# Optimization experiments

Measured on AMD Instinct MI355X. Metric: run time of the kernel, lower is better.

## Reference

```python
import jax, jax.numpy as jnp
import numpy as np

THETA = 10000.0
R_TOK = 4  # region_token_num


def _local_positions(regions, max_n):
    # 0-based position of each token within its region (count of prior tokens
    # with the same region id) -- order-based, works for any region layout.
    onehot = jax.nn.one_hot(regions, max_n + 1, dtype=jnp.int32)  # [B,T,N+1]
    counts = jnp.cumsum(onehot, axis=1)                            # inclusive
    return jnp.take_along_axis(counts, regions[..., None], axis=-1)[..., 0] - 1


def _rope(q, k, pos, theta):
    # full-head-dim rotary embedding, split-half convention
    D = q.shape[-1]
    inv_freq = 1.0 / (theta ** (jnp.arange(0, D, 2, dtype=jnp.float32) / D))  # [D/2]
    ang = pos[..., None].astype(jnp.float32) * inv_freq                        # [B,S,D/2]
    cos = jnp.tile(jnp.cos(ang), (1, 1, 2))[:, None]                           # [B,1,S,D]
    sin = jnp.tile(jnp.sin(ang), (1, 1, 2))[:, None]

    def rot(x):
        h = x.shape[-1] // 2
        return jnp.concatenate([-x[..., h:], x[..., :h]], axis=-1)

    return q * cos + rot(q) * sin, k * cos + rot(k) * sin


def setup_inputs() -> dict:
    B, H, D = 2, 16, 64
    T, MAX_N = 2048, 64
    P = MAX_N * R_TOK
    key = jax.random.key(0)
    ks = jax.random.split(key, 7)
    f = lambda k, s: jax.random.normal(k, s, dtype=jnp.float32)
    regions = jnp.sort(jax.random.randint(ks[6], (B, T), 1, MAX_N + 1, dtype=jnp.int32), axis=-1)
    return {
        'pool_q': f(ks[0], (B, H, P, D)),
        'pool_k': f(ks[1], (B, H, P, D)),
        'pool_v': f(ks[2], (B, H, P, D)),
        'x_q': f(ks[3], (B, H, T, D)),
        'x_k': f(ks[4], (B, H, T, D)),
        'x_v': f(ks[5], (B, H, T, D)),
        'regions': regions,
        't_mask': jnp.ones((B, T), dtype=bool),
        'n_mask': jnp.ones((B, MAX_N), dtype=bool),
        'max_n': MAX_N,
    }


def reference(pool_q, pool_k, pool_v, x_q, x_k, x_v, regions, t_mask, n_mask, max_n):
    B, H, P, D = pool_q.shape
    R = R_TOK
    # sequence = [pool, x]
    q = jnp.concatenate([pool_q, x_q], axis=2)
    k = jnp.concatenate([pool_k, x_k], axis=2)
    v = jnp.concatenate([pool_v, x_v], axis=2)

    # local-mode positions (use_pool_offset=False -> pool tokens at pos 0)
    pool_pos = jnp.zeros((B, P), dtype=jnp.int32)
    x_pos = (_local_positions(regions, max_n) + R) * (regions > 0).astype(jnp.int32)
    pos = jnp.concatenate([pool_pos, x_pos], axis=-1)  # [B,S]
    q, k = _rope(q, k, pos, THETA)

    # block-local (same-region) mask: [B,1,S,S], True = allowed
    pool_region = jnp.broadcast_to(jnp.repeat(jnp.arange(1, max_n + 1, dtype=jnp.int32), R)[None], (B, P))
    pool_valid = jnp.repeat(n_mask, R, axis=1)                      # [B,P]
    full_region = jnp.concatenate([pool_region, regions], axis=-1)  # [B,S]
    full_valid = jnp.concatenate([pool_valid, t_mask], axis=-1)     # [B,S]
    same = full_region[:, :, None] == full_region[:, None, :]
    valid = full_valid[:, :, None] & full_valid[:, None, :]
    nonpad = (full_region != 0)[:, :, None] & (full_region != 0)[:, None, :]
    mask = (same & valid & nonpad)[:, None]                          # [B,1,S,S]

    scores = jnp.einsum('bhqd,bhkd->bhqk', q, k) / jnp.sqrt(jnp.float32(D))
    scores = jnp.where(mask, scores, jnp.float32(-1e9))
    attn = jax.nn.softmax(scores, axis=-1)
    out = jnp.einsum('bhqk,bhkd->bhqd', attn, v)
    return out[:, :, :P, :]
```

## Files before the change

### kernel.cpp

```cpp
#include <hip/hip_runtime.h>

#define BB   2
#define HH   16
#define DD   64
#define TT   2048
#define MAXN 64
#define RTOK 4
#define PP   (MAXN * RTOK)
#define STR  72

typedef unsigned short u16x8 __attribute__((ext_vector_type(8)));
typedef unsigned short u16x4 __attribute__((ext_vector_type(4)));

__device__ __forceinline__ unsigned short f2bf(float f) {
    unsigned u = __float_as_uint(f);
    u += 0x7FFFu + ((u >> 16) & 1u);
    return (unsigned short)(u >> 16);
}
__device__ __forceinline__ float bf2f(unsigned short u) {
    return __uint_as_float(((unsigned int)u) << 16);
}

__global__ __launch_bounds__(256)
void build_ranges(const int* __restrict__ regions, int* __restrict__ tab) {
    const int b   = blockIdx.x;
    const int tid = threadIdx.x;
    const int* reg = regions + b * TT;
    int* t = tab + b * 66;
    const int i0 = tid * 8;
    int v[9];
    const int4 a0 = *(const int4*)(reg + i0);
    const int4 a1 = *(const int4*)(reg + i0 + 4);
    v[0] = a0.x; v[1] = a0.y; v[2] = a0.z; v[3] = a0.w;
    v[4] = a1.x; v[5] = a1.y; v[6] = a1.z; v[7] = a1.w;
    v[8] = (tid == 255) ? (MAXN + 1) : reg[i0 + 8];
    if (tid == 0)
        for (int rr = 1; rr <= v[0]; ++rr) t[rr] = 0;
    #pragma unroll
    for (int j = 0; j < 8; ++j)
        for (int rr = v[j] + 1; rr <= v[j + 1]; ++rr) t[rr] = i0 + j + 1;
}

__global__ __launch_bounds__(128, 4)
void lapd_attn(const float* __restrict__ pool_q,
               const float* __restrict__ pool_k,
               const float* __restrict__ pool_v,
               const float* __restrict__ x_k,
               const float* __restrict__ x_v,
               const int* __restrict__ tab,
               float* __restrict__ out) {
    const int blk   = blockIdx.x;
    const int r_idx = blk & (MAXN - 1);
    const int bh    = blk >> 6;
    const int b     = bh / HH;
    const int tid   = threadIdx.x;
    const int wave  = tid >> 6;
    const int lane  = tid & 63;

    __shared__ __align__(16) unsigned short k_s16[64][STR];
    __shared__ __align__(16) unsigned short v_t16[64][STR];
    __shared__ __align__(16) unsigned short p_s16[4][STR];
    __shared__ float q_s[4][DD];

    const int* tb    = tab + b * 66;
    const int start  = tb[r_idx + 1];
    const int cnt    = tb[r_idx + 2] - start;
    const int sstart = (cnt > 0) ? start : 0;

    const size_t poolbase = ((size_t)bh * PP + r_idx * RTOK) * DD;
    const float* pk = pool_k + poolbase;
    const float* pv = pool_v + poolbase;
    const float* xk = x_k + (size_t)bh * TT * DD;
    const float* xv = x_v + (size_t)bh * TT * DD;

    {
        const int r = lane >> 4, c = (lane & 15) * 4;
        const float4 q4 = *(const float4*)(pool_q + poolbase + (size_t)(r * DD) + c);
        *(float4*)&q_s[r][c] =
            make_float4(q4.x * 0.125f, q4.y * 0.125f, q4.z * 0.125f, q4.w * 0.125f);
    }

    const int g = lane >> 3;
    const int d = (lane & 7) * 4;
    float invf[4];
    #pragma unroll
    for (int c = 0; c < 4; ++c)
        invf[c] = __expf((float)(d + c) * (-9.210340371976184f / 32.0f));

    const int sk = lane & 31;
    const int h  = lane >> 5;
    const int row = 2 * wave + (lane >> 5);
    const int dp  = (lane & 31) * 2;

    float accA = 0.0f, accB = 0.0f, l = 0.0f;
    int xbase = 0;
    bool first = true;

    for (;;) {
        const int koff = first ? RTOK : 0;
        int nx = cnt - xbase;
        if (nx > 64 - koff) nx = 64 - koff;
        if (nx < 0) nx = 0;
        const int tn   = koff + nx;
        const int kmax = (tn + 7) & ~7;

        __syncthreads();

        #pragma unroll
        for (int ph = 0; ph < 2; ++ph) {
            const int base = 32 * wave + 16 * ph;
            if (base < tn) {
                const int keyA = base + 2 * g;
                const int keyB = keyA + 1;
                int xiA = keyA - koff; if (xiA > nx - 1) xiA = nx - 1; if (xiA < 0) xiA = 0;
                int xiB = keyB - koff; if (xiB > nx - 1) xiB = nx - 1; if (xiB < 0) xiB = 0;
                const bool pA = first && (keyA < RTOK);
                const bool pB = first && (keyB < RTOK);
                const float* kbA = pA ? (pk + keyA * DD) : (xk + (size_t)(sstart + xbase + xiA) * DD);
                const float* vbA = pA ? (pv + keyA * DD) : (xv + (size_t)(sstart + xbase + xiA) * DD);
                const float* kbB = pB ? (pk + keyB * DD) : (xk + (size_t)(sstart + xbase + xiB) * DD);
                const float* vbB = pB ? (pv + keyB * DD) : (xv + (size_t)(sstart + xbase + xiB) * DD);
                const float4 kA0 = *(const float4*)(kbA + d);
                const float4 kA1 = *(const float4*)(kbA + d + 32);
                const float4 vA0 = *(const float4*)(vbA + d);
                const float4 vA1 = *(const float4*)(vbA + d + 32);
                const float4 kB0 = *(const float4*)(kbB + d);
                const float4 kB1 = *(const float4*)(kbB + d + 32);
                const float4 vB0 = *(const float4*)(vbB + d);
                const float4 vB1 = *(const float4*)(vbB + d + 32);

                {
                    float lo0 = kA0.x, lo1 = kA0.y, lo2 = kA0.z, lo3 = kA0.w;
                    float hi0 = kA1.x, hi1 = kA1.y, hi2 = kA1.z, hi3 = kA1.w;
                    if (!pA) {
                        const float pos = (float)(xbase + xiA + RTOK);
                        float sv, cv;
                        __sincosf(pos * invf[0], &sv, &cv);
                        { const float L = lo0, H = hi0; lo0 = L*cv - H*sv; hi0 = H*cv + L*sv; }
                        __sincosf(pos * invf[1], &sv, &cv);
                        { const float L = lo1, H = hi1; lo1 = L*cv - H*sv; hi1 = H*cv + L*sv; }
                        __sincosf(pos * invf[2], &sv, &cv);
                        { const float L = lo2, H = hi2; lo2 = L*cv - H*sv; hi2 = H*cv + L*sv; }
                        __sincosf(pos * invf[3], &sv, &cv);
                        { const float L = lo3, H = hi3; lo3 = L*cv - H*sv; hi3 = H*cv + L*sv; }
                    }
                    u16x4 wlo = {f2bf(lo0), f2bf(lo1), f2bf(lo2), f2bf(lo3)};
                    u16x4 whi = {f2bf(hi0), f2bf(hi1), f2bf(hi2), f2bf(hi3)};
                    *(u16x4*)&k_s16[keyA][d]      = wlo;
                    *(u16x4*)&k_s16[keyA][d + 32] = whi;
                }
                {
                    float lo0 = kB0.x, lo1 = kB0.y, lo2 = kB0.z, lo3 = kB0.w;
                    float hi0 = kB1.x, hi1 = kB1.y, hi2 = kB1.z, hi3 = kB1.w;
                    if (!pB) {
                        const float pos = (float)(xbase + xiB + RTOK);
                        float sv, cv;
                        __sincosf(pos * invf[0], &sv, &cv);
                        { const float L = lo0, H = hi0; lo0 = L*cv - H*sv; hi0 = H*cv + L*sv; }
                        __sincosf(pos * invf[1], &sv, &cv);
                        { const float L = lo1, H = hi1; lo1 = L*cv - H*sv; hi1 = H*cv + L*sv; }
                        __sincosf(pos * invf[2], &sv, &cv);
                        { const float L = lo2, H = hi2; lo2 = L*cv - H*sv; hi2 = H*cv + L*sv; }
                        __sincosf(pos * invf[3], &sv, &cv);
                        { const float L = lo3, H = hi3; lo3 = L*cv - H*sv; hi3 = H*cv + L*sv; }
                    }
                    u16x4 wlo = {f2bf(lo0), f2bf(lo1), f2bf(lo2), f2bf(lo3)};
                    u16x4 whi = {f2bf(hi0), f2bf(hi1), f2bf(hi2), f2bf(hi3)};
                    *(u16x4*)&k_s16[keyB][d]      = wlo;
                    *(u16x4*)&k_s16[keyB][d + 32] = whi;
                }
                {
                    const unsigned w0 = (unsigned)f2bf(vA0.x) | ((unsigned)f2bf(vB0.x) << 16);
                    const unsigned w1 = (unsigned)f2bf(vA0.y) | ((unsigned)f2bf(vB0.y) << 16);
                    const unsigned w2 = (unsigned)f2bf(vA0.z) | ((unsigned)f2bf(vB0.z) << 16);
                    const unsigned w3 = (unsigned)f2bf(vA0.w) | ((unsigned)f2bf(vB0.w) << 16);
                    const unsigned h0 = (unsigned)f2bf(vA1.x) | ((unsigned)f2bf(vB1.x) << 16);
                    const unsigned h1 = (unsigned)f2bf(vA1.y) | ((unsigned)f2bf(vB1.y) << 16);
                    const unsigned h2 = (unsigned)f2bf(vA1.z) | ((unsigned)f2bf(vB1.z) << 16);
                    const unsigned h3 = (unsigned)f2bf(vA1.w) | ((unsigned)f2bf(vB1.w) << 16);
                    *(unsigned*)&v_t16[d + 0][keyA]  = w0;
                    *(unsigned*)&v_t16[d + 1][keyA]  = w1;
                    *(unsigned*)&v_t16[d + 2][keyA]  = w2;
                    *(unsigned*)&v_t16[d + 3][keyA]  = w3;
                    *(unsigned*)&v_t16[d + 32][keyA] = h0;
                    *(unsigned*)&v_t16[d + 33][keyA] = h1;
                    *(unsigned*)&v_t16[d + 34][keyA] = h2;
                    *(unsigned*)&v_t16[d + 35][keyA] = h3;
                }
            }
        }

        if (32 * wave < tn) {
            const int key = 32 * wave + sk;
            const int d0  = h * 32;
            float s0 = 0, s1 = 0, s2 = 0, s3 = 0;
            #pragma unroll
            for (int dd2 = 0; dd2 < 32; dd2 += 8) {
                const u16x8 kk = *(const u16x8*)&k_s16[key][d0 + dd2];
                const float k0 = bf2f(kk[0]), k1 = bf2f(kk[1]), k2 = bf2f(kk[2]), k3 = bf2f(kk[3]);
                const float k4 = bf2f(kk[4]), k5 = bf2f(kk[5]), k6 = bf2f(kk[6]), k7 = bf2f(kk[7]);
                const float4 qa0 = *(const float4*)&q_s[0][d0 + dd2];
                const float4 qb0 = *(const float4*)&q_s[0][d0 + dd2 + 4];
                const float4 qa1 = *(const float4*)&q_s[1][d0 + dd2];
                const float4 qb1 = *(const float4*)&q_s[1][d0 + dd2 + 4];
                const float4 qa2 = *(const float4*)&q_s[2][d0 + dd2];
                const float4 qb2 = *(const float4*)&q_s[2][d0 + dd2 + 4];
                const float4 qa3 = *(const float4*)&q_s[3][d0 + dd2];
                const float4 qb3 = *(const float4*)&q_s[3][d0 + dd2 + 4];
                s0 += qa0.x*k0 + qa0.y*k1 + qa0.z*k2 + qa0.w*k3 + qb0.x*k4 + qb0.y*k5 + qb0.z*k6 + qb0.w*k7;
                s1 += qa1.x*k0 + qa1.y*k1 + qa1.z*k2 + qa1.w*k3 + qb1.x*k4 + qb1.y*k5 + qb1.z*k6 + qb1.w*k7;
                s2 += qa2.x*k0 + qa2.y*k1 + qa2.z*k2 + qa2.w*k3 + qb2.x*k4 + qb2.y*k5 + qb2.z*k6 + qb2.w*k7;
                s3 += qa3.x*k0 + qa3.y*k1 + qa3.z*k2 + qa3.w*k3 + qb3.x*k4 + qb3.y*k5 + qb3.z*k6 + qb3.w*k7;
            }
            s0 += __shfl_xor(s0, 32, 64);
            s1 += __shfl_xor(s1, 32, 64);
            s2 += __shfl_xor(s2, 32, 64);
            s3 += __shfl_xor(s3, 32, 64);
            if (h == 0) {
                const bool ok = (key < tn);
                p_s16[0][key] = f2bf(ok ? __expf(s0) : 0.0f);
                p_s16[1][key] = f2bf(ok ? __expf(s1) : 0.0f);
                p_s16[2][key] = f2bf(ok ? __expf(s2) : 0.0f);
                p_s16[3][key] = f2bf(ok ? __expf(s3) : 0.0f);
            }
        }
        __syncthreads();

        for (int k = 0; k < kmax; k += 8) {
            const u16x8 pp = *(const u16x8*)&p_s16[row][k];
            const u16x8 w0 = *(const u16x8*)&v_t16[dp][k];
            const u16x8 w1 = *(const u16x8*)&v_t16[dp + 1][k];
            const float p0 = bf2f(pp[0]), p1 = bf2f(pp[1]), p2 = bf2f(pp[2]), p3 = bf2f(pp[3]);
            const float p4 = bf2f(pp[4]), p5 = bf2f(pp[5]), p6 = bf2f(pp[6]), p7 = bf2f(pp[7]);
            accA += p0*bf2f(w0[0]) + p1*bf2f(w0[1]) + p2*bf2f(w0[2]) + p3*bf2f(w0[3])
                  + p4*bf2f(w0[4]) + p5*bf2f(w0[5]) + p6*bf2f(w0[6]) + p7*bf2f(w0[7]);
            accB += p0*bf2f(w1[0]) + p1*bf2f(w1[1]) + p2*bf2f(w1[2]) + p3*bf2f(w1[3])
                  + p4*bf2f(w1[4]) + p5*bf2f(w1[5]) + p6*bf2f(w1[6]) + p7*bf2f(w1[7]);
            l    += ((p0 + p1) + (p2 + p3)) + ((p4 + p5) + (p6 + p7));
        }

        xbase += nx;
        first = false;
        if (xbase >= cnt) break;
    }

    const float rl = 1.0f / l;
    *(float2*)(out + poolbase + (size_t)(row * DD) + dp) = make_float2(accA * rl, accB * rl);
}

extern "C" void kernel_launch(void* const* d_in, const int* in_sizes, int n_in,
                              void* d_out, int out_size, void* d_ws, size_t ws_size,
                              hipStream_t stream) {
    const float* pool_q  = (const float*)d_in[0];
    const float* pool_k  = (const float*)d_in[1];
    const float* pool_v  = (const float*)d_in[2];
    const float* x_k     = (const float*)d_in[4];
    const float* x_v     = (const float*)d_in[5];
    const int*   regions = (const int*)d_in[6];
    float*       out     = (float*)d_out;
    int*         tab     = (int*)d_ws;

    build_ranges<<<dim3(BB), dim3(256), 0, stream>>>(regions, tab);
    lapd_attn<<<dim3(BB * HH * MAXN), dim3(128), 0, stream>>>(
        pool_q, pool_k, pool_v, x_k, x_v, tab, out);
}
```

Before: 107.8 us.

## Use 256-thread blocks with one wave per query row, dropping per-wave sync

Raises the block from 128 to 256 threads. Each of the four waves now owns one pool query row: a lane computes the full 64-dim score for one key, then one output column of P·V. Only the wave's own score row is shared, so the barrier between scoring and P·V is removed. K/V staging is spread over all 256 threads, removing the two-phase loop, and the q buffer is padded to 68 columns. The risks are more threads per tile doing duplicate q reads and a longer serial 64-element dot product per lane.

Measured after the change: 113.8 us. +5.5%, slower.

```diff
diff --git a/kernel.cpp b/kernel.cpp
--- a/kernel.cpp
+++ b/kernel.cpp
@@ -41,7 +41,7 @@
         for (int rr = v[j] + 1; rr <= v[j + 1]; ++rr) t[rr] = i0 + j + 1;
 }
 
-__global__ __launch_bounds__(128, 4)
+__global__ __launch_bounds__(256, 8)
 void lapd_attn(const float* __restrict__ pool_q,
                const float* __restrict__ pool_k,
                const float* __restrict__ pool_v,
@@ -60,7 +60,7 @@
     __shared__ __align__(16) unsigned short k_s16[64][STR];
     __shared__ __align__(16) unsigned short v_t16[64][STR];
     __shared__ __align__(16) unsigned short p_s16[4][STR];
-    __shared__ float q_s[4][DD];
+    __shared__ float q_s[4][68];
 
     const int* tb    = tab + b * 66;
     const int start  = tb[r_idx + 1];
@@ -73,26 +73,16 @@
     const float* xk = x_k + (size_t)bh * TT * DD;
     const float* xv = x_v + (size_t)bh * TT * DD;
 
-    {
-        const int r = lane >> 4, c = (lane & 15) * 4;
-        const float4 q4 = *(const float4*)(pool_q + poolbase + (size_t)(r * DD) + c);
-        *(float4*)&q_s[r][c] =
-            make_float4(q4.x * 0.125f, q4.y * 0.125f, q4.z * 0.125f, q4.w * 0.125f);
-    }
-
-    const int g = lane >> 3;
-    const int d = (lane & 7) * 4;
+    q_s[wave][lane] = pool_q[poolbase + (size_t)(wave * DD) + lane] * 0.125f;
+
+    const int g = tid >> 3;
+    const int d = (tid & 7) * 4;
     float invf[4];
     #pragma unroll
     for (int c = 0; c < 4; ++c)
         invf[c] = __expf((float)(d + c) * (-9.210340371976184f / 32.0f));
 
-    const int sk = lane & 31;
-    const int h  = lane >> 5;
-    const int row = 2 * wave + (lane >> 5);
-    const int dp  = (lane & 31) * 2;
-
-    float accA = 0.0f, accB = 0.0f, l = 0.0f;
+    float acc = 0.0f, l = 0.0f;
     int xbase = 0;
     bool first = true;
 
@@ -104,139 +94,113 @@
         const int tn   = koff + nx;
         const int kmax = (tn + 7) & ~7;
 
+        if (xbase > 0) __syncthreads();
+
+        {
+            const int keyA = 2 * g;
+            const int keyB = keyA + 1;
+            int xiA = keyA - koff; if (xiA > nx - 1) xiA = nx - 1; if (xiA < 0) xiA = 0;
+            int xiB = keyB - koff; if (xiB > nx - 1) xiB = nx - 1; if (xiB < 0) xiB = 0;
+            const bool pA = first && (keyA < RTOK);
+            const bool pB = first && (keyB < RTOK);
+            const float* kbA = pA ? (pk + keyA * DD) : (xk + (size_t)(sstart + xbase + xiA) * DD);
+            const float* vbA = pA ? (pv + keyA * DD) : (xv + (size_t)(sstart + xbase + xiA) * DD);
+            const float* kbB = pB ? (pk + keyB * DD) : (xk + (size_t)(sstart + xbase + xiB) * DD);
+            const float* vbB = pB ? (pv + keyB * DD) : (xv + (size_t)(sstart + xbase + xiB) * DD);
+            const float4 kA0 = *(const float4*)(kbA + d);
+            const float4 kA1 = *(const float4*)(kbA + d + 32);
+            const float4 vA0 = *(const float4*)(vbA + d);
+            const float4 vA1 = *(const float4*)(vbA + d + 32);
+            const float4 kB0 = *(const float4*)(kbB + d);
+            const float4 kB1 = *(const float4*)(kbB + d + 32);
+            const float4 vB0 = *(const float4*)(vbB + d);
+            const float4 vB1 = *(const float4*)(vbB + d + 32);
+
+            {
+                float lo0 = kA0.x, lo1 = kA0.y, lo2 = kA0.z, lo3 = kA0.w;
+                float hi0 = kA1.x, hi1 = kA1.y, hi2 = kA1.z, hi3 = kA1.w;
+                if (!pA) {
+                    const float pos = (float)(xbase + xiA + RTOK);
+                    float sv, cv;
+                    __sincosf(pos * invf[0], &sv, &cv);
+                    { const float L = lo0, H = hi0; lo0 = L*cv - H*sv; hi0 = H*cv + L*sv; }
+                    __sincosf(pos * invf[1], &sv, &cv);
+                    { const float L = lo1, H = hi1; lo1 = L*cv - H*sv; hi1 = H*cv + L*sv; }
+                    __sincosf(pos * invf[2], &sv, &cv);
+                    { const float L = lo2, H = hi2; lo2 = L*cv - H*sv; hi2 = H*cv + L*sv; }
+                    __sincosf(pos * invf[3], &sv, &cv);
+                    { const float L = lo3, H = hi3; lo3 = L*cv - H*sv; hi3 = H*cv + L*sv; }
+                }
+                u16x4 wlo = {f2bf(lo0), f2bf(lo1), f2bf(lo2), f2bf(lo3)};
+                u16x4 whi = {f2bf(hi0), f2bf(hi1), f2bf(hi2), f2bf(hi3)};
+                *(u16x4*)&k_s16[keyA][d]      = wlo;
+                *(u16x4*)&k_s16[keyA][d + 32] = whi;
+            }
+            {
+                float lo0 = kB0.x, lo1 = kB0.y, lo2 = kB0.z, lo3 = kB0.w;
+                float hi0 = kB1.x, hi1 = kB1.y, hi2 = kB1.z, hi3 = kB1.w;
+                if (!pB) {
+                    const float pos = (float)(xbase + xiB + RTOK);
+                    float sv, cv;
+                    __sincosf(pos * invf[0], &sv, &cv);
+                    { const float L = lo0, H = hi0; lo0 = L*cv - H*sv; hi0 = H*cv + L*sv; }
+                    __sincosf(pos * invf[1], &sv, &cv);
+                    { const float L = lo1, H = hi1; lo1 = L*cv - H*sv; hi1 = H*cv + L*sv; }
+                    __sincosf(pos * invf[2], &sv, &cv);
+                    { const float L = lo2, H = hi2; lo2 = L*cv - H*sv; hi2 = H*cv + L*sv; }
+                    __sincosf(pos * invf[3], &sv, &cv);
+                    { const float L = lo3, H = hi3; lo3 = L*cv - H*sv; hi3 = H*cv + L*sv; }
+                }
+                u16x4 wlo = {f2bf(lo0), f2bf(lo1), f2bf(lo2), f2bf(lo3)};
+                u16x4 whi = {f2bf(hi0), f2bf(hi1), f2bf(hi2), f2bf(hi3)};
+                *(u16x4*)&k_s16[keyB][d]      = wlo;
+                *(u16x4*)&k_s16[keyB][d + 32] = whi;
+            }
+            {
+                const unsigned w0 = (unsigned)f2bf(vA0.x) | ((unsigned)f2bf(vB0.x) << 16);
+                const unsigned w1 = (unsigned)f2bf(vA0.y) | ((unsigned)f2bf(vB0.y) << 16);
+                const unsigned w2 = (unsigned)f2bf(vA0.z) | ((unsigned)f2bf(vB0.z) << 16);
+                const unsigned w3 = (unsigned)f2bf(vA0.w) | ((unsigned)f2bf(vB0.w) << 16);
+                const unsigned h0 = (unsigned)f2bf(vA1.x) | ((unsigned)f2bf(vB1.x) << 16);
+                const unsigned h1 = (unsigned)f2bf(vA1.y) | ((unsigned)f2bf(vB1.y) << 16);
+                const unsigned h2 = (unsigned)f2bf(vA1.z) | ((unsigned)f2bf(vB1.z) << 16);
+                const unsigned h3 = (unsigned)f2bf(vA1.w) | ((unsigned)f2bf(vB1.w) << 16);
+                *(unsigned*)&v_t16[d + 0][keyA]  = w0;
+                *(unsigned*)&v_t16[d + 1][keyA]  = w1;
+                *(unsigned*)&v_t16[d + 2][keyA]  = w2;
+                *(unsigned*)&v_t16[d + 3][keyA]  = w3;
+                *(unsigned*)&v_t16[d + 32][keyA] = h0;
+                *(unsigned*)&v_t16[d + 33][keyA] = h1;
+                *(unsigned*)&v_t16[d + 34][keyA] = h2;
+                *(unsigned*)&v_t16[d + 35][keyA] = h3;
+            }
+        }
         __syncthreads();
 
-        #pragma unroll
-        for (int ph = 0; ph < 2; ++ph) {
-            const int base = 32 * wave + 16 * ph;
-            if (base < tn) {
-                const int keyA = base + 2 * g;
-                const int keyB = keyA + 1;
-                int xiA = keyA - koff; if (xiA > nx - 1) xiA = nx - 1; if (xiA < 0) xiA = 0;
-                int xiB = keyB - koff; if (xiB > nx - 1) xiB = nx - 1; if (xiB < 0) xiB = 0;
-                const bool pA = first && (keyA < RTOK);
-                const bool pB = first && (keyB < RTOK);
-                const float* kbA = pA ? (pk + keyA * DD) : (xk + (size_t)(sstart + xbase + xiA) * DD);
-                const float* vbA = pA ? (pv + keyA * DD) : (xv + (size_t)(sstart + xbase + xiA) * DD);
-                const float* kbB = pB ? (pk + keyB * DD) : (xk + (size_t)(sstart + xbase + xiB) * DD);
-                const float* vbB = pB ? (pv + keyB * DD) : (xv + (size_t)(sstart + xbase + xiB) * DD);
-                const float4 kA0 = *(const float4*)(kbA + d);
-                const float4 kA1 = *(const float4*)(kbA + d + 32);
-                const float4 vA0 = *(const float4*)(vbA + d);
-                const float4 vA1 = *(const float4*)(vbA + d + 32);
-                const float4 kB0 = *(const float4*)(kbB + d);
-                const float4 kB1 = *(const float4*)(kbB + d + 32);
-                const float4 vB0 = *(const float4*)(vbB + d);
-                const float4 vB1 = *(const float4*)(vbB + d + 32);
-
-                {
-                    float lo0 = kA0.x, lo1 = kA0.y, lo2 = kA0.z, lo3 = kA0.w;
-                    float hi0 = kA1.x, hi1 = kA1.y, hi2 = kA1.z, hi3 = kA1.w;
-                    if (!pA) {
-                        const float pos = (float)(xbase + xiA + RTOK);
-                        float sv, cv;
-                        __sincosf(pos * invf[0], &sv, &cv);
-                        { const float L = lo0, H = hi0; lo0 = L*cv - H*sv; hi0 = H*cv + L*sv; }
-                        __sincosf(pos * invf[1], &sv, &cv);
-                        { const float L = lo1, H = hi1; lo1 = L*cv - H*sv; hi1 = H*cv + L*sv; }
-                        __sincosf(pos * invf[2], &sv, &cv);
-                        { const float L = lo2, H = hi2; lo2 = L*cv - H*sv; hi2 = H*cv + L*sv; }
-                        __sincosf(pos * invf[3], &sv, &cv);
-                        { const float L = lo3, H = hi3; lo3 = L*cv - H*sv; hi3 = H*cv + L*sv; }
-                    }
-                    u16x4 wlo = {f2bf(lo0), f2bf(lo1), f2bf(lo2), f2bf(lo3)};
-                    u16x4 whi = {f2bf(hi0), f2bf(hi1), f2bf(hi2), f2bf(hi3)};
-                    *(u16x4*)&k_s16[keyA][d]      = wlo;
-                    *(u16x4*)&k_s16[keyA][d + 32] = whi;
-                }
-                {
-                    float lo0 = kB0.x, lo1 = kB0.y, lo2 = kB0.z, lo3 = kB0.w;
-                    float hi0 = kB1.x, hi1 = kB1.y, hi2 = kB1.z, hi3 = kB1.w;
-                    if (!pB) {
-                        const float pos = (float)(xbase + xiB + RTOK);
-                        float sv, cv;
-                        __sincosf(pos * invf[0], &sv, &cv);
-                        { const float L = lo0, H = hi0; lo0 = L*cv - H*sv; hi0 = H*cv + L*sv; }
-                        __sincosf(pos * invf[1], &sv, &cv);
-                        { const float L = lo1, H = hi1; lo1 = L*cv - H*sv; hi1 = H*cv + L*sv; }
-                        __sincosf(pos * invf[2], &sv, &cv);
-                        { const float L = lo2, H = hi2; lo2 = L*cv - H*sv; hi2 = H*cv + L*sv; }
-                        __sincosf(pos * invf[3], &sv, &cv);
-                        { const float L = lo3, H = hi3; lo3 = L*cv - H*sv; hi3 = H*cv + L*sv; }
-                    }
-                    u16x4 wlo = {f2bf(lo0), f2bf(lo1), f2bf(lo2), f2bf(lo3)};
-                    u16x4 whi = {f2bf(hi0), f2bf(hi1), f2bf(hi2), f2bf(hi3)};
-                    *(u16x4*)&k_s16[keyB][d]      = wlo;
-                    *(u16x4*)&k_s16[keyB][d + 32] = whi;
-                }
-                {
-                    const unsigned w0 = (unsigned)f2bf(vA0.x) | ((unsigned)f2bf(vB0.x) << 16);
-                    const unsigned w1 = (unsigned)f2bf(vA0.y) | ((unsigned)f2bf(vB0.y) << 16);
-                    const unsigned w2 = (unsigned)f2bf(vA0.z) | ((unsigned)f2bf(vB0.z) << 16);
-                    const unsigned w3 = (unsigned)f2bf(vA0.w) | ((unsigned)f2bf(vB0.w) << 16);
-                    const unsigned h0 = (unsigned)f2bf(vA1.x) | ((unsigned)f2bf(vB1.x) << 16);
-                    const unsigned h1 = (unsigned)f2bf(vA1.y) | ((unsigned)f2bf(vB1.y) << 16);
-                    const unsigned h2 = (unsigned)f2bf(vA1.z) | ((unsigned)f2bf(vB1.z) << 16);
-                    const unsigned h3 = (unsigned)f2bf(vA1.w) | ((unsigned)f2bf(vB1.w) << 16);
-                    *(unsigned*)&v_t16[d + 0][keyA]  = w0;
-                    *(unsigned*)&v_t16[d + 1][keyA]  = w1;
-                    *(unsigned*)&v_t16[d + 2][keyA]  = w2;
-                    *(unsigned*)&v_t16[d + 3][keyA]  = w3;
-                    *(unsigned*)&v_t16[d + 32][keyA] = h0;
-                    *(unsigned*)&v_t16[d + 33][keyA] = h1;
-                    *(unsigned*)&v_t16[d + 34][keyA] = h2;
-                    *(unsigned*)&v_t16[d + 35][keyA] = h3;
-                }
-            }
-        }
-
-        if (32 * wave < tn) {
-            const int key = 32 * wave + sk;
-            const int d0  = h * 32;
+        {
             float s0 = 0, s1 = 0, s2 = 0, s3 = 0;
             #pragma unroll
-            for (int dd2 = 0; dd2 < 32; dd2 += 8) {
-                const u16x8 kk = *(const u16x8*)&k_s16[key][d0 + dd2];
-                const float k0 = bf2f(kk[0]), k1 = bf2f(kk[1]), k2 = bf2f(kk[2]), k3 = bf2f(kk[3]);
-                const float k4 = bf2f(kk[4]), k5 = bf2f(kk[5]), k6 = bf2f(kk[6]), k7 = bf2f(kk[7]);
-                const float4 qa0 = *(const float4*)&q_s[0][d0 + dd2];
-                const float4 qb0 = *(const float4*)&q_s[0][d0 + dd2 + 4];
-                const float4 qa1 = *(const float4*)&q_s[1][d0 + dd2];
-                const float4 qb1 = *(const float4*)&q_s[1][d0 + dd2 + 4];
-                const float4 qa2 = *(const float4*)&q_s[2][d0 + dd2];
-                const float4 qb2 = *(const float4*)&q_s[2][d0 + dd2 + 4];
-                const float4 qa3 = *(const float4*)&q_s[3][d0 + dd2];
-                const float4 qb3 = *(const float4*)&q_s[3][d0 + dd2 + 4];
-                s0 += qa0.x*k0 + qa0.y*k1 + qa0.z*k2 + qa0.w*k3 + qb0.x*k4 + qb0.y*k5 + qb0.z*k6 + qb0.w*k7;
-                s1 += qa1.x*k0 + qa1.y*k1 + qa1.z*k2 + qa1.w*k3 + qb1.x*k4 + qb1.y*k5 + qb1.z*k6 + qb1.w*k7;
-                s2 += qa2.x*k0 + qa2.y*k1 + qa2.z*k2 + qa2.w*k3 + qb2.x*k4 + qb2.y*k5 + qb2.z*k6 + qb2.w*k7;
-                s3 += qa3.x*k0 + qa3.y*k1 + qa3.z*k2 + qa3.w*k3 + qb3.x*k4 + qb3.y*k5 + qb3.z*k6 + qb3.w*k7;
-            }
-            s0 += __shfl_xor(s0, 32, 64);
-            s1 += __shfl_xor(s1, 32, 64);
-            s2 += __shfl_xor(s2, 32, 64);
-            s3 += __shfl_xor(s3, 32, 64);
-            if (h == 0) {
-                const bool ok = (key < tn);
-                p_s16[0][key] = f2bf(ok ? __expf(s0) : 0.0f);
-                p_s16[1][key] = f2bf(ok ? __expf(s1) : 0.0f);
-                p_s16[2][key] = f2bf(ok ? __expf(s2) : 0.0f);
-                p_s16[3][key] = f2bf(ok ? __expf(s3) : 0.0f);
-            }
+            for (int dd2 = 0; dd2 < DD; dd2 += 8) {
+                const u16x8 kk = *(const u16x8*)&k_s16[lane][dd2];
+                const float4 qa = *(const float4*)&q_s[wave][dd2];
+                const float4 qb = *(const float4*)&q_s[wave][dd2 + 4];
+                s0 += qa.x * bf2f(kk[0]) + qb.x * bf2f(kk[4]);
+                s1 += qa.y * bf2f(kk[1]) + qb.y * bf2f(kk[5]);
+                s2 += qa.z * bf2f(kk[2]) + qb.z * bf2f(kk[6]);
+                s3 += qa.w * bf2f(kk[3]) + qb.w * bf2f(kk[7]);
+            }
+            const float s = (s0 + s1) + (s2 + s3);
+            p_s16[wave][lane] = f2bf((lane < tn) ? __expf(s) : 0.0f);
         }
-        __syncthreads();
 
         for (int k = 0; k < kmax; k += 8) {
-            const u16x8 pp = *(const u16x8*)&p_s16[row][k];
-            const u16x8 w0 = *(const u16x8*)&v_t16[dp][k];
-            const u16x8 w1 = *(const u16x8*)&v_t16[dp + 1][k];
+            const u16x8 pp = *(const u16x8*)&p_s16[wave][k];
+            const u16x8 vv = *(const u16x8*)&v_t16[lane][k];
             const float p0 = bf2f(pp[0]), p1 = bf2f(pp[1]), p2 = bf2f(pp[2]), p3 = bf2f(pp[3]);
             const float p4 = bf2f(pp[4]), p5 = bf2f(pp[5]), p6 = bf2f(pp[6]), p7 = bf2f(pp[7]);
-            accA += p0*bf2f(w0[0]) + p1*bf2f(w0[1]) + p2*bf2f(w0[2]) + p3*bf2f(w0[3])
-                  + p4*bf2f(w0[4]) + p5*bf2f(w0[5]) + p6*bf2f(w0[6]) + p7*bf2f(w0[7]);
-            accB += p0*bf2f(w1[0]) + p1*bf2f(w1[1]) + p2*bf2f(w1[2]) + p3*bf2f(w1[3])
-                  + p4*bf2f(w1[4]) + p5*bf2f(w1[5]) + p6*bf2f(w1[6]) + p7*bf2f(w1[7]);
-            l    += ((p0 + p1) + (p2 + p3)) + ((p4 + p5) + (p6 + p7));
+            acc += p0*bf2f(vv[0]) + p1*bf2f(vv[1]) + p2*bf2f(vv[2]) + p3*bf2f(vv[3])
+                 + p4*bf2f(vv[4]) + p5*bf2f(vv[5]) + p6*bf2f(vv[6]) + p7*bf2f(vv[7]);
+            l   += ((p0 + p1) + (p2 + p3)) + ((p4 + p5) + (p6 + p7));
         }
 
         xbase += nx;
@@ -244,8 +208,7 @@
         if (xbase >= cnt) break;
     }
 
-    const float rl = 1.0f / l;
-    *(float2*)(out + poolbase + (size_t)(row * DD) + dp) = make_float2(accA * rl, accB * rl);
+    out[poolbase + (size_t)(wave * DD) + lane] = acc / l;
 }
 
 extern "C" void kernel_launch(void* const* d_in, const int* in_sizes, int n_in,
@@ -261,6 +224,6 @@
     int*         tab     = (int*)d_ws;
 
     build_ranges<<<dim3(BB), dim3(256), 0, stream>>>(regions, tab);
-    lapd_attn<<<dim3(BB * HH * MAXN), dim3(128), 0, stream>>>(
+    lapd_attn<<<dim3(BB * HH * MAXN), dim3(256), 0, stream>>>(
         pool_q, pool_k, pool_v, x_k, x_v, tab, out);
 }
```
